# Optimization experiments

Hardware: AMD Instinct MI355X
Metric: run time of the kernel (lower is better)

Reference implementation:

```python
import jax, jax.numpy as jnp
import numpy as np

HID, INTER, DK = 768, 1536, 128
NEG_INF = 1.0e12
LOG512 = float(np.log(512.0))


def setup_inputs() -> dict:
    key = jax.random.key(0)
    k1, k2, k3 = jax.random.split(key, 3)
    B, S = 4, 2048
    hidden_states = jax.random.normal(k1, (B, S, HID), dtype=jnp.float32)
    attention_mask = jnp.ones((B, S), dtype=jnp.int32)
    # i_dense: hidden -> 2*INTER + DK (no bias); o_dense: INTER -> hidden (no bias)
    Wi = jax.random.normal(k2, (HID, 2 * INTER + DK), dtype=jnp.float32) * (HID ** -0.5)
    Wo = jax.random.normal(k3, (INTER, HID), dtype=jnp.float32) * (INTER ** -0.5)
    q_gamma = jnp.ones((DK,), dtype=jnp.float32)  # ScaleOffset scale, offset=False
    k_gamma = jnp.ones((DK,), dtype=jnp.float32)
    return {"hidden_states": hidden_states, "Wi": Wi, "Wo": Wo,
            "q_gamma": q_gamma, "k_gamma": k_gamma,
            "attention_mask": attention_mask}


def reference(hidden_states, Wi, Wo, q_gamma, k_gamma, attention_mask):
    # i_dense + swish, then split into u, v, qk
    x = jax.nn.silu(jnp.einsum('bsh,ho->bso', hidden_states, Wi))
    u = x[..., :INTER]
    v = x[..., INTER:2 * INTER]
    qk = x[..., 2 * INTER:]
    q = qk * q_gamma
    k = qk * k_gamma
    # single-head attention scores
    a = jnp.einsum('bmd,bnd->bmn', q, k) / (DK ** 0.5)
    mask = attention_mask[:, None, :]  # [B,1,N]
    a = jnp.where(mask == 0, -NEG_INF, a)
    l = jnp.sum(attention_mask, axis=-1, keepdims=True)[:, :, None].astype(a.dtype)  # [B,1,1]
    # softmax_plus: softmax(a * log(l) / log(512))
    A = jax.nn.softmax(a * jnp.log(l) / LOG512, axis=-1)
    # dropout inactive in eval mode
    o = jnp.einsum('bmi,ih->bmh', u * jnp.einsum('bmn,bnd->bmd', A, v), Wo)
    return o
```

## Files before the change

### kernel.cpp

```cpp
#include <hip/hip_runtime.h>
#include <hip/hip_bf16.h>
#include <math.h>

#define BATCH 4
#define SEQ   2048
#define HID   768
#define INTER 1536
#define DK    128
#define NTOT  3200
#define MROWS 8192
#define LN512 6.2383246250395075f

typedef _Float16 half8  __attribute__((ext_vector_type(8)));
typedef float    floatx4 __attribute__((ext_vector_type(4)));

typedef const __attribute__((address_space(1))) unsigned int* gas1_t;
typedef __attribute__((address_space(3))) unsigned int* las3_t;

static __device__ __forceinline__ void load16(const _Float16* g, _Float16* l) {
    __builtin_amdgcn_global_load_lds((gas1_t)g, (las3_t)l, 16, 0, 0);
}
#define WAIT_VM(N)    asm volatile("s_waitcnt vmcnt(" #N ")" ::: "memory")
#define WAIT_LGKM0()  asm volatile("s_waitcnt lgkmcnt(0)" ::: "memory")
#define BARRIER_RAW() asm volatile("s_barrier" ::: "memory")

__global__ void cast_h_kernel(const float* __restrict__ in, _Float16* __restrict__ out, int n) {
    int i = (blockIdx.x * blockDim.x + threadIdx.x) * 8;
    if (i < n) {
        float4 a = *reinterpret_cast<const float4*>(in + i);
        float4 b = *reinterpret_cast<const float4*>(in + i + 4);
        half8 h = {(_Float16)a.x, (_Float16)a.y, (_Float16)a.z, (_Float16)a.w,
                   (_Float16)b.x, (_Float16)b.y, (_Float16)b.z, (_Float16)b.w};
        *reinterpret_cast<half8*>(out + i) = h;
    }
}

__global__ void trans_wi_kernel(const float* __restrict__ Wi, _Float16* __restrict__ WiT) {
    __shared__ _Float16 tile[32][33];
    const int c0 = blockIdx.x * 32, r0 = blockIdx.y * 32;
    const int tx = threadIdx.x, ty = threadIdx.y;
#pragma unroll
    for (int j = 0; j < 32; j += 8)
        tile[tx][ty + j] = (_Float16)Wi[(size_t)(r0 + ty + j) * NTOT + c0 + tx];
    __syncthreads();
#pragma unroll
    for (int j = 0; j < 32; j += 8)
        WiT[(size_t)(c0 + ty + j) * HID + r0 + tx] = tile[ty + j][tx];
}

__global__ void trans_wo_kernel(const float* __restrict__ Wo, _Float16* __restrict__ WoT) {
    __shared__ _Float16 tile[32][33];
    const int c0 = blockIdx.x * 32, r0 = blockIdx.y * 32;
    const int tx = threadIdx.x, ty = threadIdx.y;
#pragma unroll
    for (int j = 0; j < 32; j += 8)
        tile[tx][ty + j] = (_Float16)Wo[(size_t)(r0 + ty + j) * HID + c0 + tx];
    __syncthreads();
#pragma unroll
    for (int j = 0; j < 32; j += 8)
        WoT[(size_t)(c0 + ty + j) * INTER + r0 + tx] = tile[ty + j][tx];
}

__global__ void mask_scales_kernel(const int* __restrict__ mask, float* __restrict__ scales) {
    __shared__ int sh[256];
    int b = blockIdx.x;
    int s = 0;
    for (int i = threadIdx.x; i < SEQ; i += 256) s += mask[b * SEQ + i];
    sh[threadIdx.x] = s;
    __syncthreads();
    for (int off = 128; off > 0; off >>= 1) {
        if (threadIdx.x < off) sh[threadIdx.x] += sh[threadIdx.x + off];
        __syncthreads();
    }
    if (threadIdx.x == 0) scales[b] = logf((float)sh[0]) / LN512;
}

struct TileCtx {
    int tid, wave, lane, quad, l16, wm, wn, c0, c1, sw;
};
static __device__ __forceinline__ TileCtx make_ctx() {
    TileCtx t;
    t.tid = threadIdx.x;
    t.wave = t.tid >> 6; t.lane = t.tid & 63;
    t.quad = t.lane >> 4; t.l16 = t.lane & 15;
    t.wm = (t.wave & 1) * 64;
    t.wn = (t.wave >> 1) * 64;
    t.c0 = t.tid;
    t.c1 = t.tid + 256;
    t.sw = (t.l16 >> 1) & 3;
    return t;
}

static __device__ __forceinline__ void gemm_mainloop_3s(
    const TileCtx& t,
    const _Float16* __restrict__ Ag, int lda,
    const _Float16* __restrict__ Bg, int ldb,
    int K, _Float16* smem, floatx4 acc[4][4])
{
    const int ar0 = t.c0 >> 2, ak0 = ((t.c0 & 3) ^ ((t.c0 >> 3) & 3)) * 8;
    const int ar1 = t.c1 >> 2, ak1 = ((t.c1 & 3) ^ ((t.c1 >> 3) & 3)) * 8;
    const _Float16* a0 = Ag + (size_t)ar0 * lda + ak0;
    const _Float16* a1 = Ag + (size_t)ar1 * lda + ak1;
    const _Float16* b0 = Bg + (size_t)ar0 * ldb + ak0;
    const _Float16* b1 = Bg + (size_t)ar1 * ldb + ak1;
    _Float16* Asl = smem + t.c0 * 8;
    _Float16* Bsl = smem + 12288 + t.c0 * 8;
    const int nIter = K >> 5;

    const int qsw = (t.quad ^ t.sw) * 8;

    load16(a0, Asl);        load16(a1, Asl + 2048);
    load16(b0, Bsl);        load16(b1, Bsl + 2048);
    if (nIter > 1) {
        load16(a0 + 32, Asl + 4096); load16(a1 + 32, Asl + 6144);
        load16(b0 + 32, Bsl + 4096); load16(b1 + 32, Bsl + 6144);
    }

    int sc = 0;
    int sp = 2;
    for (int k = 0; k < nIter; ++k) {
        if (k + 1 < nIter) {
            WAIT_VM(4);
        } else {
            WAIT_VM(0);
        }
        BARRIER_RAW();
        if (k + 2 < nIter) {
            const int off = sp * 4096;
            const int k0 = (k + 2) << 5;
            load16(a0 + k0, Asl + off); load16(a1 + k0, Asl + off + 2048);
            load16(b0 + k0, Bsl + off); load16(b1 + k0, Bsl + off + 2048);
        }
        const _Float16* Ab = smem + sc * 4096;
        const _Float16* Bb = smem + 12288 + sc * 4096;
        half8 af[4], bf[4];
#pragma unroll
        for (int mt = 0; mt < 4; ++mt)
            af[mt] = *reinterpret_cast<const half8*>(Ab + (t.wm + mt * 16 + t.l16) * 32 + qsw);
#pragma unroll
        for (int nt = 0; nt < 4; ++nt)
            bf[nt] = *reinterpret_cast<const half8*>(Bb + (t.wn + nt * 16 + t.l16) * 32 + qsw);
#pragma unroll
        for (int mt = 0; mt < 4; ++mt)
#pragma unroll
            for (int nt = 0; nt < 4; ++nt)
                acc[mt][nt] = __builtin_amdgcn_mfma_f32_16x16x32_f16(af[mt], bf[nt], acc[mt][nt], 0, 0, 0);
        WAIT_LGKM0();
        sc = (sc == 2) ? 0 : sc + 1;
        sp = (sp == 2) ? 0 : sp + 1;
    }
}

__global__ __launch_bounds__(256) void gemm1_kernel(
    const _Float16* __restrict__ Hb, const _Float16* __restrict__ WiT,
    const float* __restrict__ qg, const float* __restrict__ kg,
    _Float16* __restrict__ u, _Float16* __restrict__ vT,
    _Float16* __restrict__ q, _Float16* __restrict__ k)
{
    __shared__ _Float16 smem[24576];
    TileCtx t = make_ctx();
    const int f = blockIdx.x;
    const int xcd = f & 7, i = f >> 3;
    const int m0 = ((xcd << 3) | (i & 7)) * 128;
    const int n0 = (i >> 3) * 128;

    floatx4 acc[4][4] = {};
    gemm_mainloop_3s(t, Hb + (size_t)m0 * HID, HID, WiT + (size_t)n0 * HID, HID, HID, smem, acc);

    if (n0 >= INTER && n0 < 2 * INTER) {
        __syncthreads();
        const int bb = m0 >> 11, sloc = m0 & (SEQ - 1), cI = n0 - INTER;
#pragma unroll
        for (int mt = 0; mt < 4; ++mt) {
#pragma unroll
            for (int nt = 0; nt < 4; ++nt) {
                int c = t.wn + nt * 16 + t.l16;
#pragma unroll
                for (int i2 = 0; i2 < 4; ++i2) {
                    int r = t.wm + mt * 16 + t.quad * 4 + i2;
                    float x = acc[mt][nt][i2];
                    float y = x / (1.0f + __expf(-x));
                    smem[c * 128 + (r ^ ((c & 15) << 3))] = (_Float16)y;
                }
            }
        }
        __syncthreads();
#pragma unroll
        for (int p = 0; p < 8; ++p) {
            int chunk = t.tid + p * 256;
            int cl = chunk >> 4, sc = chunk & 15;
            int scs = sc ^ (cl & 15);
            half8 v = *reinterpret_cast<const half8*>(smem + cl * 128 + scs * 8);
            *reinterpret_cast<half8*>(vT + ((size_t)bb * INTER + cI + cl) * SEQ + sloc + sc * 8) = v;
        }
    } else {
#pragma unroll
        for (int mt = 0; mt < 4; ++mt) {
#pragma unroll
            for (int nt = 0; nt < 4; ++nt) {
                int col = n0 + t.wn + nt * 16 + t.l16;
#pragma unroll
                for (int i2 = 0; i2 < 4; ++i2) {
                    int row = m0 + t.wm + mt * 16 + t.quad * 4 + i2;
                    float x = acc[mt][nt][i2];
                    float y = x / (1.0f + __expf(-x));
                    if (n0 < INTER) {
                        u[(size_t)row * INTER + col] = (_Float16)y;
                    } else {
                        int c = col - 2 * INTER;
                        q[(size_t)row * DK + c] = (_Float16)(y * qg[c]);
                        k[(size_t)row * DK + c] = (_Float16)(y * kg[c]);
                    }
                }
            }
        }
    }
}

__global__ __launch_bounds__(256) void scores_kernel(
    const _Float16* __restrict__ q, const _Float16* __restrict__ k,
    const int* __restrict__ mask, const float* __restrict__ scales,
    _Float16* __restrict__ P)
{
    const int b = blockIdx.y;
    const int m0 = blockIdx.x * 16;
    const int tid = threadIdx.x;
    const int wave = tid >> 6, lane = tid & 63, quad = lane >> 4, l16 = lane & 15;
    const float scale = scales[b];

    half8 aq[4];
    const _Float16* qrow = q + (b * SEQ + m0 + l16) * DK + quad * 8;
#pragma unroll
    for (int kk = 0; kk < 4; ++kk) aq[kk] = *reinterpret_cast<const half8*>(qrow + kk * 32);

    floatx4 sc[32];
#pragma unroll
    for (int nt = 0; nt < 32; ++nt) {
        int n0 = nt * 64 + wave * 16;
        const _Float16* krow = k + (b * SEQ + n0 + l16) * DK + quad * 8;
        floatx4 acc = {};
#pragma unroll
        for (int kk = 0; kk < 4; ++kk) {
            half8 bq = *reinterpret_cast<const half8*>(krow + kk * 32);
            acc = __builtin_amdgcn_mfma_f32_16x16x32_f16(aq[kk], bq, acc, 0, 0, 0);
        }
        sc[nt] = acc;
    }

    const float rs = 0.08838834764831845f * scale;
    const float mval = -1e12f * scale;
    float rmax[4] = {-3.4e38f, -3.4e38f, -3.4e38f, -3.4e38f};
#pragma unroll
    for (int nt = 0; nt < 32; ++nt) {
        int ncol = nt * 64 + wave * 16 + l16;
        bool mok = mask[b * SEQ + ncol] != 0;
#pragma unroll
        for (int i = 0; i < 4; ++i) {
            float s = mok ? sc[nt][i] * rs : mval;
            sc[nt][i] = s;
            rmax[i] = fmaxf(rmax[i], s);
        }
    }
#pragma unroll
    for (int i = 0; i < 4; ++i) {
#pragma unroll
        for (int off = 1; off < 16; off <<= 1)
            rmax[i] = fmaxf(rmax[i], __shfl_xor(rmax[i], off, 64));
    }
    __shared__ float redmax[4][16];
    __shared__ float redsum[4][16];
    if (l16 == 0) {
#pragma unroll
        for (int i = 0; i < 4; ++i) redmax[wave][quad * 4 + i] = rmax[i];
    }
    __syncthreads();
#pragma unroll
    for (int i = 0; i < 4; ++i) {
        int r = quad * 4 + i;
        rmax[i] = fmaxf(fmaxf(redmax[0][r], redmax[1][r]), fmaxf(redmax[2][r], redmax[3][r]));
    }
    float rsum[4] = {0.f, 0.f, 0.f, 0.f};
#pragma unroll
    for (int nt = 0; nt < 32; ++nt) {
#pragma unroll
        for (int i = 0; i < 4; ++i) {
            float e = __expf(sc[nt][i] - rmax[i]);
            sc[nt][i] = e;
            rsum[i] += e;
        }
    }
#pragma unroll
    for (int i = 0; i < 4; ++i) {
#pragma unroll
        for (int off = 1; off < 16; off <<= 1) rsum[i] += __shfl_xor(rsum[i], off, 64);
    }
    if (l16 == 0) {
#pragma unroll
        for (int i = 0; i < 4; ++i) redsum[wave][quad * 4 + i] = rsum[i];
    }
    __syncthreads();
#pragma unroll
    for (int i = 0; i < 4; ++i) {
        int r = quad * 4 + i;
        float tot = redsum[0][r] + redsum[1][r] + redsum[2][r] + redsum[3][r];
        float inv = 1.0f / tot;
        int row = m0 + r;
        _Float16* Prow = P + ((size_t)b * SEQ + row) * SEQ;
#pragma unroll
        for (int nt = 0; nt < 32; ++nt) {
            int ncol = nt * 64 + wave * 16 + l16;
            Prow[ncol] = (_Float16)(sc[nt][i] * inv);
        }
    }
}

__global__ __launch_bounds__(256) void pv_kernel(
    const _Float16* __restrict__ P, const _Float16* __restrict__ vT,
    _Float16* __restrict__ u)
{
    __shared__ _Float16 smem[24576];
    TileCtx t = make_ctx();
    const int f = blockIdx.x;
    const int xcd = f & 7, i = f >> 3;
    const int b = i / 24, j = i % 24;
    const int m0 = (xcd * 2 + (j & 1)) * 128;
    const int n0 = (j >> 1) * 128;
    const _Float16* Pb  = P  + (size_t)b * SEQ * SEQ;
    const _Float16* vTb = vT + (size_t)b * INTER * SEQ;

    floatx4 acc[4][4] = {};
    gemm_mainloop_3s(t, Pb + (size_t)m0 * SEQ, SEQ, vTb + (size_t)n0 * SEQ, SEQ, SEQ, smem, acc);

#pragma unroll
    for (int mt = 0; mt < 4; ++mt) {
#pragma unroll
        for (int nt = 0; nt < 4; ++nt) {
            int col = n0 + t.wn + nt * 16 + t.l16;
#pragma unroll
            for (int i2 = 0; i2 < 4; ++i2) {
                int row = m0 + t.wm + mt * 16 + t.quad * 4 + i2;
                size_t gidx = ((size_t)(b * SEQ + row)) * INTER + col;
                float uv = (float)u[gidx];
                u[gidx] = (_Float16)(acc[mt][nt][i2] * uv);
            }
        }
    }
}

__global__ __launch_bounds__(256) void gemm2_kernel(
    const _Float16* __restrict__ tin, const _Float16* __restrict__ WoT,
    float* __restrict__ out)
{
    __shared__ _Float16 smem[24576];
    TileCtx t = make_ctx();
    const int f = blockIdx.x;
    const int xcd = f & 7, i = f >> 3;
    const int m0 = ((xcd << 3) | (i & 7)) * 128;
    const int n0 = (i >> 3) * 128;

    floatx4 acc[4][4] = {};
    gemm_mainloop_3s(t, tin + (size_t)m0 * INTER, INTER, WoT + (size_t)n0 * INTER, INTER, INTER, smem, acc);

#pragma unroll
    for (int mt = 0; mt < 4; ++mt) {
#pragma unroll
        for (int nt = 0; nt < 4; ++nt) {
            int col = n0 + t.wn + nt * 16 + t.l16;
#pragma unroll
            for (int i2 = 0; i2 < 4; ++i2) {
                int row = m0 + t.wm + mt * 16 + t.quad * 4 + i2;
                out[(size_t)row * HID + col] = acc[mt][nt][i2];
            }
        }
    }
}

extern "C" void kernel_launch(void* const* d_in, const int* in_sizes, int n_in,
                              void* d_out, int out_size, void* d_ws, size_t ws_size,
                              hipStream_t stream) {
    const float* H    = (const float*)d_in[0];
    const float* Wi   = (const float*)d_in[1];
    const float* Wo   = (const float*)d_in[2];
    const float* qg   = (const float*)d_in[3];
    const float* kg   = (const float*)d_in[4];
    const int*   mask = (const int*)d_in[5];
    float* out = (float*)d_out;

    char* base = (char*)d_ws;
    size_t off = 0;
    auto alloc = [&](size_t bytes) { void* p = base + off; off = (off + bytes + 255) & ~(size_t)255; return p; };
    _Float16* Hb   = (_Float16*)alloc((size_t)MROWS * HID * 2);
    _Float16* WiT  = (_Float16*)alloc((size_t)NTOT * HID * 2);
    _Float16* WoT  = (_Float16*)alloc((size_t)HID * INTER * 2);
    _Float16* u    = (_Float16*)alloc((size_t)MROWS * INTER * 2);
    _Float16* vT   = (_Float16*)alloc((size_t)BATCH * INTER * SEQ * 2);
    _Float16* q    = (_Float16*)alloc((size_t)MROWS * DK * 2);
    _Float16* k    = (_Float16*)alloc((size_t)MROWS * DK * 2);
    _Float16* P    = (_Float16*)alloc((size_t)BATCH * SEQ * SEQ * 2);
    float*    scales = (float*)alloc(4 * sizeof(float));

    {
        int n = MROWS * HID;
        cast_h_kernel<<<n / 8 / 256, 256, 0, stream>>>(H, Hb, n);
        trans_wi_kernel<<<dim3(NTOT / 32, HID / 32), dim3(32, 8), 0, stream>>>(Wi, WiT);
        trans_wo_kernel<<<dim3(HID / 32, INTER / 32), dim3(32, 8), 0, stream>>>(Wo, WoT);
        mask_scales_kernel<<<BATCH, 256, 0, stream>>>(mask, scales);
    }
    gemm1_kernel<<<1600, 256, 0, stream>>>(Hb, WiT, qg, kg, u, vT, q, k);
    {
        dim3 grid(SEQ / 16, BATCH);
        scores_kernel<<<grid, 256, 0, stream>>>(q, k, mask, scales, P);
    }
    pv_kernel<<<768, 256, 0, stream>>>(P, vT, u);
    gemm2_kernel<<<384, 256, 0, stream>>>(u, WoT, out);
}
```

Baseline: 310.8 us.

## Use 32x32x16 MFMA in PV and output GEMMs; remap scores grid per XCD

```diff
diff --git a/kernel.cpp b/kernel.cpp
--- a/kernel.cpp
+++ b/kernel.cpp
@@ -11,8 +11,9 @@
 #define MROWS 8192
 #define LN512 6.2383246250395075f
 
-typedef _Float16 half8  __attribute__((ext_vector_type(8)));
+typedef _Float16 half8   __attribute__((ext_vector_type(8)));
 typedef float    floatx4 __attribute__((ext_vector_type(4)));
+typedef float    floatx16 __attribute__((ext_vector_type(16)));
 
 typedef const __attribute__((address_space(1))) unsigned int* gas1_t;
 typedef __attribute__((address_space(3))) unsigned int* las3_t;
@@ -76,22 +77,22 @@
 }
 
 struct TileCtx {
-    int tid, wave, lane, quad, l16, wm, wn, c0, c1, sw;
+    int tid, wave, lane, quad, l16, l31, half, wm, wn, c0, c1;
 };
 static __device__ __forceinline__ TileCtx make_ctx() {
     TileCtx t;
     t.tid = threadIdx.x;
     t.wave = t.tid >> 6; t.lane = t.tid & 63;
     t.quad = t.lane >> 4; t.l16 = t.lane & 15;
+    t.l31 = t.lane & 31;  t.half = t.lane >> 5;
     t.wm = (t.wave & 1) * 64;
     t.wn = (t.wave >> 1) * 64;
     t.c0 = t.tid;
     t.c1 = t.tid + 256;
-    t.sw = (t.l16 >> 1) & 3;
     return t;
 }
 
-static __device__ __forceinline__ void gemm_mainloop_3s(
+static __device__ __forceinline__ void gemm_mainloop_3s16(
     const TileCtx& t,
     const _Float16* __restrict__ Ag, int lda,
     const _Float16* __restrict__ Bg, int ldb,
@@ -106,8 +107,8 @@
     _Float16* Asl = smem + t.c0 * 8;
     _Float16* Bsl = smem + 12288 + t.c0 * 8;
     const int nIter = K >> 5;
-
-    const int qsw = (t.quad ^ t.sw) * 8;
+    const int sw = (t.l16 >> 1) & 3;
+    const int qsw = (t.quad ^ sw) * 8;
 
     load16(a0, Asl);        load16(a1, Asl + 2048);
     load16(b0, Bsl);        load16(b1, Bsl + 2048);
@@ -116,14 +117,9 @@
         load16(b0 + 32, Bsl + 4096); load16(b1 + 32, Bsl + 6144);
     }
 
-    int sc = 0;
-    int sp = 2;
+    int sc = 0, sp = 2;
     for (int k = 0; k < nIter; ++k) {
-        if (k + 1 < nIter) {
-            WAIT_VM(4);
-        } else {
-            WAIT_VM(0);
-        }
+        if (k + 1 < nIter) { WAIT_VM(4); } else { WAIT_VM(0); }
         BARRIER_RAW();
         if (k + 2 < nIter) {
             const int off = sp * 4096;
@@ -151,6 +147,71 @@
     }
 }
 
+static __device__ __forceinline__ void gemm_mainloop_3s32(
+    const TileCtx& t,
+    const _Float16* __restrict__ Ag, int lda,
+    const _Float16* __restrict__ Bg, int ldb,
+    int K, _Float16* smem, floatx16 acc[2][2])
+{
+    const int r0i = t.c0 >> 2, s0 = (((r0i >> 1) ^ (r0i >> 3)) & 3);
+    const int r1i = t.c1 >> 2, s1 = (((r1i >> 1) ^ (r1i >> 3)) & 3);
+    const int ak0 = ((t.c0 & 3) ^ s0) * 8;
+    const int ak1 = ((t.c1 & 3) ^ s1) * 8;
+    const _Float16* a0 = Ag + (size_t)r0i * lda + ak0;
+    const _Float16* a1 = Ag + (size_t)r1i * lda + ak1;
+    const _Float16* b0 = Bg + (size_t)r0i * ldb + ak0;
+    const _Float16* b1 = Bg + (size_t)r1i * ldb + ak1;
+    _Float16* Asl = smem + t.c0 * 8;
+    _Float16* Bsl = smem + 12288 + t.c0 * 8;
+    const int nIter = K >> 5;
+
+    const int fsw = ((t.l31 >> 1) ^ (t.l31 >> 3)) & 3;
+
+    load16(a0, Asl);        load16(a1, Asl + 2048);
+    load16(b0, Bsl);        load16(b1, Bsl + 2048);
+    if (nIter > 1) {
+        load16(a0 + 32, Asl + 4096); load16(a1 + 32, Asl + 6144);
+        load16(b0 + 32, Bsl + 4096); load16(b1 + 32, Bsl + 6144);
+    }
+
+    int sc = 0, sp = 2;
+    for (int k = 0; k < nIter; ++k) {
+        if (k + 1 < nIter) { WAIT_VM(4); } else { WAIT_VM(0); }
+        BARRIER_RAW();
+        if (k + 2 < nIter) {
+            const int off = sp * 4096;
+            const int k0 = (k + 2) << 5;
+            load16(a0 + k0, Asl + off); load16(a1 + k0, Asl + off + 2048);
+            load16(b0 + k0, Bsl + off); load16(b1 + k0, Bsl + off + 2048);
+        }
+        const _Float16* Ab = smem + sc * 4096;
+        const _Float16* Bb = smem + 12288 + sc * 4096;
+        half8 af[2][2], bf[2][2];
+#pragma unroll
+        for (int mt = 0; mt < 2; ++mt)
+#pragma unroll
+            for (int h = 0; h < 2; ++h)
+                af[mt][h] = *reinterpret_cast<const half8*>(
+                    Ab + (t.wm + mt * 32 + t.l31) * 32 + (((h * 2 + t.half) ^ fsw) * 8));
+#pragma unroll
+        for (int nt = 0; nt < 2; ++nt)
+#pragma unroll
+            for (int h = 0; h < 2; ++h)
+                bf[nt][h] = *reinterpret_cast<const half8*>(
+                    Bb + (t.wn + nt * 32 + t.l31) * 32 + (((h * 2 + t.half) ^ fsw) * 8));
+#pragma unroll
+        for (int h = 0; h < 2; ++h)
+#pragma unroll
+            for (int mt = 0; mt < 2; ++mt)
+#pragma unroll
+                for (int nt = 0; nt < 2; ++nt)
+                    acc[mt][nt] = __builtin_amdgcn_mfma_f32_32x32x16_f16(af[mt][h], bf[nt][h], acc[mt][nt], 0, 0, 0);
+        WAIT_LGKM0();
+        sc = (sc == 2) ? 0 : sc + 1;
+        sp = (sp == 2) ? 0 : sp + 1;
+    }
+}
+
 __global__ __launch_bounds__(256) void gemm1_kernel(
     const _Float16* __restrict__ Hb, const _Float16* __restrict__ WiT,
     const float* __restrict__ qg, const float* __restrict__ kg,
@@ -165,7 +226,7 @@
     const int n0 = (i >> 3) * 128;
 
     floatx4 acc[4][4] = {};
-    gemm_mainloop_3s(t, Hb + (size_t)m0 * HID, HID, WiT + (size_t)n0 * HID, HID, HID, smem, acc);
+    gemm_mainloop_3s16(t, Hb + (size_t)m0 * HID, HID, WiT + (size_t)n0 * HID, HID, HID, smem, acc);
 
     if (n0 >= INTER && n0 < 2 * INTER) {
         __syncthreads();
@@ -222,8 +283,10 @@
     const int* __restrict__ mask, const float* __restrict__ scales,
     _Float16* __restrict__ P)
 {
-    const int b = blockIdx.y;
-    const int m0 = blockIdx.x * 16;
+    const int f = blockIdx.x;
+    const int xcd = f & 7, i = f >> 3;
+    const int b = xcd >> 1;
+    const int m0 = ((xcd & 1) * 64 + i) * 16;
     const int tid = threadIdx.x;
     const int wave = tid >> 6, lane = tid & 63, quad = lane >> 4, l16 = lane & 15;
     const float scale = scales[b];
@@ -255,53 +318,53 @@
         int ncol = nt * 64 + wave * 16 + l16;
         bool mok = mask[b * SEQ + ncol] != 0;
 #pragma unroll
-        for (int i = 0; i < 4; ++i) {
-            float s = mok ? sc[nt][i] * rs : mval;
-            sc[nt][i] = s;
-            rmax[i] = fmaxf(rmax[i], s);
-        }
-    }
-#pragma unroll
-    for (int i = 0; i < 4; ++i) {
+        for (int i2 = 0; i2 < 4; ++i2) {
+            float s = mok ? sc[nt][i2] * rs : mval;
+            sc[nt][i2] = s;
+            rmax[i2] = fmaxf(rmax[i2], s);
+        }
+    }
+#pragma unroll
+    for (int i2 = 0; i2 < 4; ++i2) {
 #pragma unroll
         for (int off = 1; off < 16; off <<= 1)
-            rmax[i] = fmaxf(rmax[i], __shfl_xor(rmax[i], off, 64));
+            rmax[i2] = fmaxf(rmax[i2], __shfl_xor(rmax[i2], off, 64));
     }
     __shared__ float redmax[4][16];
     __shared__ float redsum[4][16];
     if (l16 == 0) {
 #pragma unroll
-        for (int i = 0; i < 4; ++i) redmax[wave][quad * 4 + i] = rmax[i];
+        for (int i2 = 0; i2 < 4; ++i2) redmax[wave][quad * 4 + i2] = rmax[i2];
     }
     __syncthreads();
 #pragma unroll
-    for (int i = 0; i < 4; ++i) {
-        int r = quad * 4 + i;
-        rmax[i] = fmaxf(fmaxf(redmax[0][r], redmax[1][r]), fmaxf(redmax[2][r], redmax[3][r]));
+    for (int i2 = 0; i2 < 4; ++i2) {
+        int r = quad * 4 + i2;
+        rmax[i2] = fmaxf(fmaxf(redmax[0][r], redmax[1][r]), fmaxf(redmax[2][r], redmax[3][r]));
     }
     float rsum[4] = {0.f, 0.f, 0.f, 0.f};
 #pragma unroll
     for (int nt = 0; nt < 32; ++nt) {
 #pragma unroll
-        for (int i = 0; i < 4; ++i) {
-            float e = __expf(sc[nt][i] - rmax[i]);
-            sc[nt][i] = e;
-            rsum[i] += e;
-        }
-    }
-#pragma unroll
-    for (int i = 0; i < 4; ++i) {
-#pragma unroll
-        for (int off = 1; off < 16; off <<= 1) rsum[i] += __shfl_xor(rsum[i], off, 64);
+        for (int i2 = 0; i2 < 4; ++i2) {
+            float e = __expf(sc[nt][i2] - rmax[i2]);
+            sc[nt][i2] = e;
+            rsum[i2] += e;
+        }
+    }
+#pragma unroll
+    for (int i2 = 0; i2 < 4; ++i2) {
+#pragma unroll
+        for (int off = 1; off < 16; off <<= 1) rsum[i2] += __shfl_xor(rsum[i2], off, 64);
     }
     if (l16 == 0) {
 #pragma unroll
-        for (int i = 0; i < 4; ++i) redsum[wave][quad * 4 + i] = rsum[i];
+        for (int i2 = 0; i2 < 4; ++i2) redsum[wave][quad * 4 + i2] = rsum[i2];
     }
     __syncthreads();
 #pragma unroll
-    for (int i = 0; i < 4; ++i) {
-        int r = quad * 4 + i;
+    for (int i2 = 0; i2 < 4; ++i2) {
+        int r = quad * 4 + i2;
         float tot = redsum[0][r] + redsum[1][r] + redsum[2][r] + redsum[3][r];
         float inv = 1.0f / tot;
         int row = m0 + r;
@@ -309,7 +372,7 @@
 #pragma unroll
         for (int nt = 0; nt < 32; ++nt) {
             int ncol = nt * 64 + wave * 16 + l16;
-            Prow[ncol] = (_Float16)(sc[nt][i] * inv);
+            Prow[ncol] = (_Float16)(sc[nt][i2] * inv);
         }
     }
 }
@@ -328,20 +391,20 @@
     const _Float16* Pb  = P  + (size_t)b * SEQ * SEQ;
     const _Float16* vTb = vT + (size_t)b * INTER * SEQ;
 
-    floatx4 acc[4][4] = {};
-    gemm_mainloop_3s(t, Pb + (size_t)m0 * SEQ, SEQ, vTb + (size_t)n0 * SEQ, SEQ, SEQ, smem, acc);
-
-#pragma unroll
-    for (int mt = 0; mt < 4; ++mt) {
-#pragma unroll
-        for (int nt = 0; nt < 4; ++nt) {
-            int col = n0 + t.wn + nt * 16 + t.l16;
-#pragma unroll
-            for (int i2 = 0; i2 < 4; ++i2) {
-                int row = m0 + t.wm + mt * 16 + t.quad * 4 + i2;
+    floatx16 acc[2][2] = {};
+    gemm_mainloop_3s32(t, Pb + (size_t)m0 * SEQ, SEQ, vTb + (size_t)n0 * SEQ, SEQ, SEQ, smem, acc);
+
+#pragma unroll
+    for (int mt = 0; mt < 2; ++mt) {
+#pragma unroll
+        for (int nt = 0; nt < 2; ++nt) {
+            int col = n0 + t.wn + nt * 32 + t.l31;
+#pragma unroll
+            for (int reg = 0; reg < 16; ++reg) {
+                int row = m0 + t.wm + mt * 32 + (reg & 3) + 8 * (reg >> 2) + 4 * t.half;
                 size_t gidx = ((size_t)(b * SEQ + row)) * INTER + col;
                 float uv = (float)u[gidx];
-                u[gidx] = (_Float16)(acc[mt][nt][i2] * uv);
+                u[gidx] = (_Float16)(acc[mt][nt][reg] * uv);
             }
         }
     }
@@ -358,18 +421,18 @@
     const int m0 = ((xcd << 3) | (i & 7)) * 128;
     const int n0 = (i >> 3) * 128;
 
-    floatx4 acc[4][4] = {};
-    gemm_mainloop_3s(t, tin + (size_t)m0 * INTER, INTER, WoT + (size_t)n0 * INTER, INTER, INTER, smem, acc);
-
-#pragma unroll
-    for (int mt = 0; mt < 4; ++mt) {
-#pragma unroll
-        for (int nt = 0; nt < 4; ++nt) {
-            int col = n0 + t.wn + nt * 16 + t.l16;
-#pragma unroll
-            for (int i2 = 0; i2 < 4; ++i2) {
-                int row = m0 + t.wm + mt * 16 + t.quad * 4 + i2;
-                out[(size_t)row * HID + col] = acc[mt][nt][i2];
+    floatx16 acc[2][2] = {};
+    gemm_mainloop_3s32(t, tin + (size_t)m0 * INTER, INTER, WoT + (size_t)n0 * INTER, INTER, INTER, smem, acc);
+
+#pragma unroll
+    for (int mt = 0; mt < 2; ++mt) {
+#pragma unroll
+        for (int nt = 0; nt < 2; ++nt) {
+            int col = n0 + t.wn + nt * 32 + t.l31;
+#pragma unroll
+            for (int reg = 0; reg < 16; ++reg) {
+                int row = m0 + t.wm + mt * 32 + (reg & 3) + 8 * (reg >> 2) + 4 * t.half;
+                out[(size_t)row * HID + col] = acc[mt][nt][reg];
             }
         }
     }
@@ -407,10 +470,7 @@
         mask_scales_kernel<<<BATCH, 256, 0, stream>>>(mask, scales);
     }
     gemm1_kernel<<<1600, 256, 0, stream>>>(Hb, WiT, qg, kg, u, vT, q, k);
-    {
-        dim3 grid(SEQ / 16, BATCH);
-        scores_kernel<<<grid, 256, 0, stream>>>(q, k, mask, scales, P);
-    }
+    scores_kernel<<<512, 256, 0, stream>>>(q, k, mask, scales, P);
     pv_kernel<<<768, 256, 0, stream>>>(P, vT, u);
     gemm2_kernel<<<384, 256, 0, stream>>>(u, WoT, out);
 }
```

New measurement: 307.7 us. About the same (-1.0%).
